# Optimization experiments

Hardware: AMD Instinct MI355X
Metric: run time of the kernel (lower is better)

Reference implementation:

```python
import jax, jax.numpy as jnp
import numpy as np

D_MODEL = 512
NUM_HEADS = 8
DEPTH = D_MODEL // NUM_HEADS


def setup_inputs() -> dict:
    key = jax.random.key(0)
    kx, kq, kk, kv, ko = jax.random.split(key, 5)
    scale = 1.0 / np.sqrt(D_MODEL)
    return {
        "x": jax.random.normal(kx, (4, 2048, D_MODEL), dtype=jnp.float32),
        "W_q": jax.random.normal(kq, (D_MODEL, D_MODEL), dtype=jnp.float32) * scale,
        "W_k": jax.random.normal(kk, (D_MODEL, D_MODEL), dtype=jnp.float32) * scale,
        "W_v": jax.random.normal(kv, (D_MODEL, D_MODEL), dtype=jnp.float32) * scale,
        "W_o": jax.random.normal(ko, (D_MODEL, D_MODEL), dtype=jnp.float32) * scale,
    }


def reference(x, W_q, W_k, W_v, W_o):
    B, S, _ = x.shape
    # nn.Linear with weight W: y = x @ W.T
    def split_heads(t):
        return t.reshape(B, S, NUM_HEADS, DEPTH).transpose(0, 2, 1, 3)  # [B,H,S,D]
    Q = split_heads(x @ W_q.T)
    K = split_heads(x @ W_k.T)
    V = split_heads(x @ W_v.T)
    b = -jnp.log(jnp.asarray(S, dtype=jnp.float32))  # -log(seq_len) bias
    inv_sqrt_dk = 1.0 / jnp.sqrt(jnp.asarray(DEPTH, dtype=jnp.float32))
    qk = jnp.einsum('bhqd,bhkd->bhqk', Q, K) * inv_sqrt_dk
    attn = jax.nn.sigmoid(qk + b)  # non-softmax sigmoid attention
    out = jnp.einsum('bhqk,bhkd->bhqd', attn, V)
    out = out.transpose(0, 2, 1, 3).reshape(B, S, D_MODEL)
    return out @ W_o.T
```

## Files before the change

kernel.cpp:

```cpp
#include <hip/hip_runtime.h>
#include <stdint.h>

typedef __bf16 bf16x8 __attribute__((ext_vector_type(8)));
typedef float f32x4 __attribute__((ext_vector_type(4)));
typedef unsigned short us4 __attribute__((ext_vector_type(4)));

#define SEQ 2048
#define NHEADS 8

#define GLOAD_LDS16(gp, lp)                                                        \
  __builtin_amdgcn_global_load_lds(                                                \
      (const __attribute__((address_space(1))) void*)(uintptr_t)(const void*)(gp), \
      (__attribute__((address_space(3))) void*)(uintptr_t)(void*)(lp), 16, 0, 0)

__device__ __forceinline__ unsigned short f2bf(float f) {
  unsigned int u = __builtin_bit_cast(unsigned int, f);
  u += 0x7fffu + ((u >> 16) & 1u);
  return (unsigned short)(u >> 16);
}

__global__ void cvt_kernel(const float* __restrict__ src,
                           unsigned short* __restrict__ dst, int n4) {
  int i = blockIdx.x * blockDim.x + threadIdx.x;
  if (i >= n4) return;
  float4 v = ((const float4*)src)[i];
  us4 o;
  o.x = f2bf(v.x); o.y = f2bf(v.y); o.z = f2bf(v.z); o.w = f2bf(v.w);
  ((us4*)dst)[i] = o;
}

__device__ __forceinline__ void gemm_tile_bt(const unsigned short* __restrict__ A,
                                             const unsigned short* __restrict__ B,
                                             int m0, int n0,
                                             unsigned short* As, unsigned short* Bs,
                                             f32x4 (&acc)[4][4]) {
  const int tid = threadIdx.x;
  const int w = tid >> 6, lane = tid & 63;
  const int wr = w >> 1, wc = w & 1;
  const int lrow = lane & 15, q = lane >> 4;
  const int snb = w * 32 + (lane >> 3);
  const int scb = lane & 7;

#pragma unroll
  for (int i = 0; i < 4; ++i)
#pragma unroll
    for (int j = 0; j < 4; ++j)
#pragma unroll
      for (int r = 0; r < 4; ++r) acc[i][j][r] = 0.f;

  for (int kt = 0; kt < 8; ++kt) {
    __syncthreads();
#pragma unroll
    for (int t = 0; t < 4; ++t) {
      int n = snb + t * 8;
      int cbg = scb ^ (n & 7);
      GLOAD_LDS16(A + (size_t)(m0 + n) * 512 + kt * 64 + cbg * 8,
                  As + (w * 32 + t * 8) * 64);
      GLOAD_LDS16(B + (size_t)(n0 + n) * 512 + kt * 64 + cbg * 8,
                  Bs + (w * 32 + t * 8) * 64);
    }
    __syncthreads();

    bf16x8 af[4][2], bfr[4][2];
#pragma unroll
    for (int i = 0; i < 4; ++i) {
      int m = wr * 64 + i * 16 + lrow;
#pragma unroll
      for (int kk = 0; kk < 2; ++kk) {
        int cb = (kk * 4 + q) ^ (m & 7);
        af[i][kk] = *(const bf16x8*)(As + m * 64 + cb * 8);
      }
    }
#pragma unroll
    for (int j = 0; j < 4; ++j) {
      int n = wc * 64 + j * 16 + lrow;
#pragma unroll
      for (int kk = 0; kk < 2; ++kk) {
        int cb = (kk * 4 + q) ^ (n & 7);
        bfr[j][kk] = *(const bf16x8*)(Bs + n * 64 + cb * 8);
      }
    }
#pragma unroll
    for (int i = 0; i < 4; ++i)
#pragma unroll
      for (int j = 0; j < 4; ++j) {
        acc[i][j] = __builtin_amdgcn_mfma_f32_16x16x32_bf16(af[i][0], bfr[j][0], acc[i][j], 0, 0, 0);
        acc[i][j] = __builtin_amdgcn_mfma_f32_16x16x32_bf16(af[i][1], bfr[j][1], acc[i][j], 0, 0, 0);
      }
  }
}

__global__ __launch_bounds__(256, 2) void qkv_kernel(
    const unsigned short* __restrict__ A, const unsigned short* __restrict__ Wq,
    const unsigned short* __restrict__ Wk, const unsigned short* __restrict__ Wv,
    unsigned short* __restrict__ Qo, unsigned short* __restrict__ Ko,
    unsigned short* __restrict__ Vto) {
  __shared__ unsigned short As[128 * 64];
  __shared__ unsigned short Bs[128 * 64];
  const int m0 = blockIdx.x * 128, n0 = blockIdx.y * 128, z = blockIdx.z;
  const unsigned short* Bp = (z == 0) ? Wq : (z == 1) ? Wk : Wv;
  f32x4 acc[4][4];
  gemm_tile_bt(A, Bp, m0, n0, As, Bs, acc);

  const int tid = threadIdx.x, w = tid >> 6, lane = tid & 63;
  const int wr = w >> 1, wc = w & 1, lcol = lane & 15, q = lane >> 4;
  if (z < 2) {
    unsigned short* outp = (z == 0) ? Qo : Ko;
#pragma unroll
    for (int i = 0; i < 4; ++i) {
      int gm0 = m0 + wr * 64 + i * 16 + q * 4;
#pragma unroll
      for (int j = 0; j < 4; ++j) {
        int gn = n0 + wc * 64 + j * 16 + lcol;
        int h = gn >> 6, d = gn & 63;
#pragma unroll
        for (int r = 0; r < 4; ++r) {
          int gm = gm0 + r;
          int b = gm >> 11, s = gm & 2047;
          outp[(((size_t)(b * NHEADS + h) * SEQ + s) << 6) + d] = f2bf(acc[i][j][r]);
        }
      }
    }
  } else {
#pragma unroll
    for (int i = 0; i < 4; ++i) {
      int gm0 = m0 + wr * 64 + i * 16 + q * 4;
      int b = gm0 >> 11, s0 = gm0 & 2047;
#pragma unroll
      for (int j = 0; j < 4; ++j) {
        int gn = n0 + wc * 64 + j * 16 + lcol;
        int h = gn >> 6, d = gn & 63;
        us4 v;
        v.x = f2bf(acc[i][j][0]); v.y = f2bf(acc[i][j][1]);
        v.z = f2bf(acc[i][j][2]); v.w = f2bf(acc[i][j][3]);
        *(us4*)(Vto + ((size_t)(b * NHEADS + h) * 64 + d) * SEQ + s0) = v;
      }
    }
  }
}

__global__ __launch_bounds__(256, 2) void attn_kernel(
    const unsigned short* __restrict__ Qw, const unsigned short* __restrict__ Kw,
    const unsigned short* __restrict__ Vtw, unsigned short* __restrict__ Ow) {
  __shared__ unsigned short lds[32768];
  unsigned short* Ks = lds;
  unsigned short* Vts = lds + 8192;
  unsigned short* Ps = lds + 16384;
  unsigned short* Qs = Ps;

  const int tid = threadIdx.x, w = tid >> 6, lane = tid & 63;
  const int wr = w >> 1, wc = w & 1, lrow = lane & 15, q = lane >> 4;
  const int bh = blockIdx.y, q0 = blockIdx.x * 128;
  const unsigned short* Qp = Qw + ((size_t)bh * SEQ + q0) * 64;
  const unsigned short* Kp = Kw + (size_t)bh * SEQ * 64;
  const unsigned short* Vp = Vtw + (size_t)bh * 64 * SEQ;

  const int snb = w * 32 + (lane >> 3), scb = lane & 7;
  const int vnb = w * 16 + (lane >> 4), vcb = lane & 15;

#pragma unroll
  for (int t = 0; t < 4; ++t) {
    int n = snb + t * 8;
    int cbg = scb ^ (n & 7);
    GLOAD_LDS16(Qp + (size_t)n * 64 + cbg * 8, Qs + (w * 32 + t * 8) * 64);
  }
  __syncthreads();

  bf16x8 qa[4][2];
#pragma unroll
  for (int i = 0; i < 4; ++i) {
    int m = wr * 64 + i * 16 + lrow;
#pragma unroll
    for (int kk = 0; kk < 2; ++kk) {
      int cb = (kk * 4 + q) ^ (m & 7);
      qa[i][kk] = *(const bf16x8*)(Qs + m * 64 + cb * 8);
    }
  }

  f32x4 oacc[4][2];
#pragma unroll
  for (int i = 0; i < 4; ++i)
#pragma unroll
    for (int j = 0; j < 2; ++j)
#pragma unroll
      for (int r = 0; r < 4; ++r) oacc[i][j][r] = 0.f;

  const float c1 = -0.18033688011112042f;

  for (int kt = 0; kt < 16; ++kt) {
    __syncthreads();
#pragma unroll
    for (int t = 0; t < 4; ++t) {
      int n = snb + t * 8;
      int cbg = scb ^ (n & 7);
      GLOAD_LDS16(Kp + (size_t)(kt * 128 + n) * 64 + cbg * 8, Ks + (w * 32 + t * 8) * 64);
    }
#pragma unroll
    for (int t = 0; t < 4; ++t) {
      int n = vnb + t * 4;
      int cbg = vcb ^ (n & 15);
      GLOAD_LDS16(Vp + (size_t)n * SEQ + kt * 128 + cbg * 8, Vts + (w * 16 + t * 4) * 128);
    }
    __syncthreads();

    f32x4 sacc[4][4];
#pragma unroll
    for (int i = 0; i < 4; ++i)
#pragma unroll
      for (int j = 0; j < 4; ++j)
#pragma unroll
        for (int r = 0; r < 4; ++r) sacc[i][j][r] = 0.f;
    bf16x8 kb[4][2];
#pragma unroll
    for (int j = 0; j < 4; ++j) {
      int n = wc * 64 + j * 16 + lrow;
#pragma unroll
      for (int kk = 0; kk < 2; ++kk) {
        int cb = (kk * 4 + q) ^ (n & 7);
        kb[j][kk] = *(const bf16x8*)(Ks + n * 64 + cb * 8);
      }
    }
#pragma unroll
    for (int i = 0; i < 4; ++i)
#pragma unroll
      for (int j = 0; j < 4; ++j) {
        sacc[i][j] = __builtin_amdgcn_mfma_f32_16x16x32_bf16(qa[i][0], kb[j][0], sacc[i][j], 0, 0, 0);
        sacc[i][j] = __builtin_amdgcn_mfma_f32_16x16x32_bf16(qa[i][1], kb[j][1], sacc[i][j], 0, 0, 0);
      }

#pragma unroll
    for (int i = 0; i < 4; ++i) {
      int prow0 = wr * 64 + i * 16 + q * 4;
#pragma unroll
      for (int j = 0; j < 4; ++j) {
        int pcol = wc * 64 + j * 16 + lrow;
        int cb = pcol >> 3, ci = pcol & 7;
#pragma unroll
        for (int r = 0; r < 4; ++r) {
          int prow = prow0 + r;
          float e = __builtin_amdgcn_exp2f(__builtin_fmaf(sacc[i][j][r], c1, 11.0f));
          float p = __builtin_amdgcn_rcpf(1.0f + e);
          Ps[prow * 128 + ((cb ^ (prow & 15)) * 8) + ci] = f2bf(p);
        }
      }
    }
    __syncthreads();

#pragma unroll
    for (int ks = 0; ks < 4; ++ks) {
      bf16x8 pa[4], vb[2];
#pragma unroll
      for (int i2 = 0; i2 < 4; ++i2) {
        int m = wr * 64 + i2 * 16 + lrow;
        int cb = (ks * 4 + q) ^ (m & 15);
        pa[i2] = *(const bf16x8*)(Ps + m * 128 + cb * 8);
      }
#pragma unroll
      for (int j2 = 0; j2 < 2; ++j2) {
        int n = wc * 32 + j2 * 16 + lrow;
        int cb = (ks * 4 + q) ^ (n & 15);
        vb[j2] = *(const bf16x8*)(Vts + n * 128 + cb * 8);
      }
#pragma unroll
      for (int i2 = 0; i2 < 4; ++i2)
#pragma unroll
        for (int j2 = 0; j2 < 2; ++j2)
          oacc[i2][j2] = __builtin_amdgcn_mfma_f32_16x16x32_bf16(pa[i2], vb[j2], oacc[i2][j2], 0, 0, 0);
    }
  }

  const int b = bh >> 3, h = bh & 7;
#pragma unroll
  for (int i2 = 0; i2 < 4; ++i2) {
#pragma unroll
    for (int j2 = 0; j2 < 2; ++j2) {
      int d = wc * 32 + j2 * 16 + lrow;
#pragma unroll
      for (int r = 0; r < 4; ++r) {
        int row = wr * 64 + i2 * 16 + q * 4 + r;
        int s = q0 + row;
        Ow[((size_t)(b * SEQ + s) * NHEADS + h) * 64 + d] = f2bf(oacc[i2][j2][r]);
      }
    }
  }
}

__global__ __launch_bounds__(256, 2) void oproj_kernel(
    const unsigned short* __restrict__ A, const unsigned short* __restrict__ Wo,
    float* __restrict__ out) {
  __shared__ unsigned short As[128 * 64];
  __shared__ unsigned short Bs[128 * 64];
  const int m0 = blockIdx.x * 128, n0 = blockIdx.y * 128;
  f32x4 acc[4][4];
  gemm_tile_bt(A, Wo, m0, n0, As, Bs, acc);

  const int tid = threadIdx.x, w = tid >> 6, lane = tid & 63;
  const int wr = w >> 1, wc = w & 1, lcol = lane & 15, q = lane >> 4;
#pragma unroll
  for (int i = 0; i < 4; ++i) {
    int gm0 = m0 + wr * 64 + i * 16 + q * 4;
#pragma unroll
    for (int j = 0; j < 4; ++j) {
      int gn = n0 + wc * 64 + j * 16 + lcol;
#pragma unroll
      for (int r = 0; r < 4; ++r)
        out[(size_t)(gm0 + r) * 512 + gn] = acc[i][j][r];
    }
  }
}

extern "C" void kernel_launch(void* const* d_in, const int* in_sizes, int n_in,
                              void* d_out, int out_size, void* d_ws, size_t ws_size,
                              hipStream_t stream) {
  const float* x = (const float*)d_in[0];
  const float* Wq = (const float*)d_in[1];
  const float* Wk = (const float*)d_in[2];
  const float* Wv = (const float*)d_in[3];
  const float* Wo = (const float*)d_in[4];
  float* out = (float*)d_out;
  char* ws = (char*)d_ws;

  unsigned short* xb  = (unsigned short*)(ws + 0);
  unsigned short* wqb = (unsigned short*)(ws + 8388608);
  unsigned short* wkb = (unsigned short*)(ws + 8912896);
  unsigned short* wvb = (unsigned short*)(ws + 9437184);
  unsigned short* wob = (unsigned short*)(ws + 9961472);
  unsigned short* Qw  = (unsigned short*)(ws + 10485760);
  unsigned short* Kw  = (unsigned short*)(ws + 18874368);
  unsigned short* Vtw = (unsigned short*)(ws + 27262976);
  unsigned short* Ow  = (unsigned short*)(ws + 35651584);

  cvt_kernel<<<4096, 256, 0, stream>>>(x, xb, 4194304 / 4);
  cvt_kernel<<<256, 256, 0, stream>>>(Wq, wqb, 262144 / 4);
  cvt_kernel<<<256, 256, 0, stream>>>(Wk, wkb, 262144 / 4);
  cvt_kernel<<<256, 256, 0, stream>>>(Wv, wvb, 262144 / 4);
  cvt_kernel<<<256, 256, 0, stream>>>(Wo, wob, 262144 / 4);

  qkv_kernel<<<dim3(64, 4, 3), 256, 0, stream>>>(xb, wqb, wkb, wvb, Qw, Kw, Vtw);
  attn_kernel<<<dim3(16, 32), 256, 0, stream>>>(Qw, Kw, Vtw, Ow);
  oproj_kernel<<<dim3(64, 4), 256, 0, stream>>>(Ow, wob, out);
}
```

Baseline: 177.0 us.

## Switch pipeline to fp16, shrink attention tiles, remap grid per XCD, merge weight casts

Converts every intermediate from bf16 to fp16, using packed RTZ conversion and fp16 MFMA. Q and K are now stored token-major with stride 512, and the QK GEMM is computed in transposed form. The attention kernel moves to 64-row query tiles with smaller LDS (P aliases K) to allow 4 blocks per CU, uses a 1-D grid mapped so each XCD handles contiguous heads for L2 reuse, and replaces the sigmoid's rcp with a scaled exp plus polynomial correction. The four weight conversion launches are merged into one. Risks include fp16 range/precision issues and the accuracy of the sigmoid approximation, which assumes the exponential term stays small.

```diff
diff --git a/kernel.cpp b/kernel.cpp
--- a/kernel.cpp
+++ b/kernel.cpp
@@ -1,9 +1,10 @@
 #include <hip/hip_runtime.h>
 #include <stdint.h>
 
-typedef __bf16 bf16x8 __attribute__((ext_vector_type(8)));
+typedef _Float16 f16x8 __attribute__((ext_vector_type(8)));
+typedef _Float16 f16x4 __attribute__((ext_vector_type(4)));
+typedef __fp16 h16x2 __attribute__((ext_vector_type(2)));
 typedef float f32x4 __attribute__((ext_vector_type(4)));
-typedef unsigned short us4 __attribute__((ext_vector_type(4)));
 
 #define SEQ 2048
 #define NHEADS 8
@@ -13,26 +14,36 @@
       (const __attribute__((address_space(1))) void*)(uintptr_t)(const void*)(gp), \
       (__attribute__((address_space(3))) void*)(uintptr_t)(void*)(lp), 16, 0, 0)
 
-__device__ __forceinline__ unsigned short f2bf(float f) {
-  unsigned int u = __builtin_bit_cast(unsigned int, f);
-  u += 0x7fffu + ((u >> 16) & 1u);
-  return (unsigned short)(u >> 16);
-}
-
-__global__ void cvt_kernel(const float* __restrict__ src,
-                           unsigned short* __restrict__ dst, int n4) {
+__device__ __forceinline__ f16x4 pack4(float a, float b, float c, float d) {
+  h16x2 lo = __builtin_amdgcn_cvt_pkrtz(a, b);
+  h16x2 hi = __builtin_amdgcn_cvt_pkrtz(c, d);
+  f16x4 o;
+  o.x = (_Float16)lo.x; o.y = (_Float16)lo.y;
+  o.z = (_Float16)hi.x; o.w = (_Float16)hi.y;
+  return o;
+}
+
+__global__ void cvt_x_kernel(const float* __restrict__ src,
+                             _Float16* __restrict__ dst, int n4) {
   int i = blockIdx.x * blockDim.x + threadIdx.x;
   if (i >= n4) return;
   float4 v = ((const float4*)src)[i];
-  us4 o;
-  o.x = f2bf(v.x); o.y = f2bf(v.y); o.z = f2bf(v.z); o.w = f2bf(v.w);
-  ((us4*)dst)[i] = o;
-}
-
-__device__ __forceinline__ void gemm_tile_bt(const unsigned short* __restrict__ A,
-                                             const unsigned short* __restrict__ B,
+  ((f16x4*)dst)[i] = pack4(v.x, v.y, v.z, v.w);
+}
+
+__global__ void cvt_w_kernel(const float* __restrict__ w0, const float* __restrict__ w1,
+                             const float* __restrict__ w2, const float* __restrict__ w3,
+                             _Float16* __restrict__ dst) {
+  const float* s = (blockIdx.y == 0) ? w0 : (blockIdx.y == 1) ? w1 : (blockIdx.y == 2) ? w2 : w3;
+  int i = blockIdx.x * 256 + threadIdx.x;
+  float4 v = ((const float4*)s)[i];
+  ((f16x4*)(dst + (size_t)blockIdx.y * 262144))[i] = pack4(v.x, v.y, v.z, v.w);
+}
+
+__device__ __forceinline__ void gemm_tile_bt(const _Float16* __restrict__ A,
+                                             const _Float16* __restrict__ B,
                                              int m0, int n0,
-                                             unsigned short* As, unsigned short* Bs,
+                                             _Float16* As, _Float16* Bs,
                                              f32x4 (&acc)[4][4]) {
   const int tid = threadIdx.x;
   const int w = tid >> 6, lane = tid & 63;
@@ -61,14 +72,14 @@
     }
     __syncthreads();
 
-    bf16x8 af[4][2], bfr[4][2];
+    f16x8 af[4][2], bfr[4][2];
 #pragma unroll
     for (int i = 0; i < 4; ++i) {
       int m = wr * 64 + i * 16 + lrow;
 #pragma unroll
       for (int kk = 0; kk < 2; ++kk) {
         int cb = (kk * 4 + q) ^ (m & 7);
-        af[i][kk] = *(const bf16x8*)(As + m * 64 + cb * 8);
+        af[i][kk] = *(const f16x8*)(As + m * 64 + cb * 8);
       }
     }
 #pragma unroll
@@ -77,160 +88,160 @@
 #pragma unroll
       for (int kk = 0; kk < 2; ++kk) {
         int cb = (kk * 4 + q) ^ (n & 7);
-        bfr[j][kk] = *(const bf16x8*)(Bs + n * 64 + cb * 8);
+        bfr[j][kk] = *(const f16x8*)(Bs + n * 64 + cb * 8);
       }
     }
 #pragma unroll
     for (int i = 0; i < 4; ++i)
 #pragma unroll
       for (int j = 0; j < 4; ++j) {
-        acc[i][j] = __builtin_amdgcn_mfma_f32_16x16x32_bf16(af[i][0], bfr[j][0], acc[i][j], 0, 0, 0);
-        acc[i][j] = __builtin_amdgcn_mfma_f32_16x16x32_bf16(af[i][1], bfr[j][1], acc[i][j], 0, 0, 0);
+        acc[i][j] = __builtin_amdgcn_mfma_f32_16x16x32_f16(af[i][0], bfr[j][0], acc[i][j], 0, 0, 0);
+        acc[i][j] = __builtin_amdgcn_mfma_f32_16x16x32_f16(af[i][1], bfr[j][1], acc[i][j], 0, 0, 0);
       }
   }
 }
 
 __global__ __launch_bounds__(256, 2) void qkv_kernel(
-    const unsigned short* __restrict__ A, const unsigned short* __restrict__ Wq,
-    const unsigned short* __restrict__ Wk, const unsigned short* __restrict__ Wv,
-    unsigned short* __restrict__ Qo, unsigned short* __restrict__ Ko,
-    unsigned short* __restrict__ Vto) {
-  __shared__ unsigned short As[128 * 64];
-  __shared__ unsigned short Bs[128 * 64];
-  const int m0 = blockIdx.x * 128, n0 = blockIdx.y * 128, z = blockIdx.z;
-  const unsigned short* Bp = (z == 0) ? Wq : (z == 1) ? Wk : Wv;
+    const _Float16* __restrict__ xb, const _Float16* __restrict__ Wq,
+    const _Float16* __restrict__ Wk, const _Float16* __restrict__ Wv,
+    _Float16* __restrict__ Qo, _Float16* __restrict__ Ko, _Float16* __restrict__ Vto) {
+  __shared__ _Float16 As[128 * 64];
+  __shared__ _Float16 Bs[128 * 64];
+  const int z = blockIdx.z;
   f32x4 acc[4][4];
-  gemm_tile_bt(A, Bp, m0, n0, As, Bs, acc);
-
   const int tid = threadIdx.x, w = tid >> 6, lane = tid & 63;
   const int wr = w >> 1, wc = w & 1, lcol = lane & 15, q = lane >> 4;
+
   if (z < 2) {
-    unsigned short* outp = (z == 0) ? Qo : Ko;
+    const int m0 = blockIdx.y * 128;
+    const int n0 = blockIdx.x * 128;
+    gemm_tile_bt((z == 0) ? Wq : Wk, xb, m0, n0, As, Bs, acc);
+    _Float16* outp = (z == 0) ? Qo : Ko;
 #pragma unroll
     for (int i = 0; i < 4; ++i) {
-      int gm0 = m0 + wr * 64 + i * 16 + q * 4;
-#pragma unroll
-      for (int j = 0; j < 4; ++j) {
-        int gn = n0 + wc * 64 + j * 16 + lcol;
-        int h = gn >> 6, d = gn & 63;
-#pragma unroll
-        for (int r = 0; r < 4; ++r) {
-          int gm = gm0 + r;
-          int b = gm >> 11, s = gm & 2047;
-          outp[(((size_t)(b * NHEADS + h) * SEQ + s) << 6) + d] = f2bf(acc[i][j][r]);
-        }
+      int c0 = m0 + wr * 64 + i * 16 + q * 4;
+#pragma unroll
+      for (int j = 0; j < 4; ++j) {
+        int s = n0 + wc * 64 + j * 16 + lcol;
+        *(f16x4*)(outp + (size_t)s * 512 + c0) =
+            pack4(acc[i][j][0], acc[i][j][1], acc[i][j][2], acc[i][j][3]);
       }
     }
   } else {
+    const int m0 = blockIdx.x * 128;
+    const int n0 = blockIdx.y * 128;
+    gemm_tile_bt(xb, Wv, m0, n0, As, Bs, acc);
 #pragma unroll
     for (int i = 0; i < 4; ++i) {
-      int gm0 = m0 + wr * 64 + i * 16 + q * 4;
-      int b = gm0 >> 11, s0 = gm0 & 2047;
-#pragma unroll
-      for (int j = 0; j < 4; ++j) {
-        int gn = n0 + wc * 64 + j * 16 + lcol;
-        int h = gn >> 6, d = gn & 63;
-        us4 v;
-        v.x = f2bf(acc[i][j][0]); v.y = f2bf(acc[i][j][1]);
-        v.z = f2bf(acc[i][j][2]); v.w = f2bf(acc[i][j][3]);
-        *(us4*)(Vto + ((size_t)(b * NHEADS + h) * 64 + d) * SEQ + s0) = v;
-      }
-    }
-  }
-}
-
-__global__ __launch_bounds__(256, 2) void attn_kernel(
-    const unsigned short* __restrict__ Qw, const unsigned short* __restrict__ Kw,
-    const unsigned short* __restrict__ Vtw, unsigned short* __restrict__ Ow) {
-  __shared__ unsigned short lds[32768];
-  unsigned short* Ks = lds;
-  unsigned short* Vts = lds + 8192;
-  unsigned short* Ps = lds + 16384;
-  unsigned short* Qs = Ps;
+      int s0 = m0 + wr * 64 + i * 16 + q * 4;
+      int b = s0 >> 11, sl = s0 & 2047;
+#pragma unroll
+      for (int j = 0; j < 4; ++j) {
+        int c = n0 + wc * 64 + j * 16 + lcol;
+        int h = c >> 6, d = c & 63;
+        *(f16x4*)(Vto + ((size_t)((b * NHEADS + h) * 64 + d)) * SEQ + sl) =
+            pack4(acc[i][j][0], acc[i][j][1], acc[i][j][2], acc[i][j][3]);
+      }
+    }
+  }
+}
+
+__global__ __launch_bounds__(256, 4) void attn_kernel(
+    const _Float16* __restrict__ Qw, const _Float16* __restrict__ Kw,
+    const _Float16* __restrict__ Vtw, _Float16* __restrict__ Ow) {
+  __shared__ _Float16 lds[20480];
+  _Float16* Ks = lds;
+  _Float16* Qs = lds + 8192;
+  _Float16* Vts = lds + 12288;
+  _Float16* Ps = lds;
 
   const int tid = threadIdx.x, w = tid >> 6, lane = tid & 63;
   const int wr = w >> 1, wc = w & 1, lrow = lane & 15, q = lane >> 4;
-  const int bh = blockIdx.y, q0 = blockIdx.x * 128;
-  const unsigned short* Qp = Qw + ((size_t)bh * SEQ + q0) * 64;
-  const unsigned short* Kp = Kw + (size_t)bh * SEQ * 64;
-  const unsigned short* Vp = Vtw + (size_t)bh * 64 * SEQ;
-
-  const int snb = w * 32 + (lane >> 3), scb = lane & 7;
-  const int vnb = w * 16 + (lane >> 4), vcb = lane & 15;
-
-#pragma unroll
-  for (int t = 0; t < 4; ++t) {
-    int n = snb + t * 8;
-    int cbg = scb ^ (n & 7);
-    GLOAD_LDS16(Qp + (size_t)n * 64 + cbg * 8, Qs + (w * 32 + t * 8) * 64);
+
+  const int L = blockIdx.x;
+  const int xcd = L & 7, slot = L >> 3;
+  const int bh = xcd * 4 + (slot >> 5), qt = slot & 31;
+  const int b = bh >> 3, h = bh & 7;
+
+  const _Float16* Qp = Qw + ((size_t)(b * SEQ + qt * 64)) * 512 + h * 64;
+  const _Float16* Kp = Kw + ((size_t)b * SEQ) * 512 + h * 64;
+  const _Float16* Vp = Vtw + (size_t)bh * 64 * SEQ;
+
+#pragma unroll
+  for (int t = 0; t < 2; ++t) {
+    int n = w * 16 + t * 8 + (lane >> 3);
+    int cbg = (lane & 7) ^ (n & 7);
+    GLOAD_LDS16(Qp + (size_t)n * 512 + cbg * 8, Qs + (w * 16 + t * 8) * 64);
   }
   __syncthreads();
 
-  bf16x8 qa[4][2];
-#pragma unroll
-  for (int i = 0; i < 4; ++i) {
-    int m = wr * 64 + i * 16 + lrow;
+  f16x8 qa[2][2];
+#pragma unroll
+  for (int i = 0; i < 2; ++i) {
+    int m = wr * 32 + i * 16 + lrow;
 #pragma unroll
     for (int kk = 0; kk < 2; ++kk) {
       int cb = (kk * 4 + q) ^ (m & 7);
-      qa[i][kk] = *(const bf16x8*)(Qs + m * 64 + cb * 8);
-    }
-  }
-
-  f32x4 oacc[4][2];
-#pragma unroll
-  for (int i = 0; i < 4; ++i)
+      qa[i][kk] = *(const f16x8*)(Qs + m * 64 + cb * 8);
+    }
+  }
+
+  f32x4 oacc[2][2];
+#pragma unroll
+  for (int i = 0; i < 2; ++i)
 #pragma unroll
     for (int j = 0; j < 2; ++j)
 #pragma unroll
       for (int r = 0; r < 4; ++r) oacc[i][j][r] = 0.f;
 
-  const float c1 = -0.18033688011112042f;
+  const float c1 = 0.18033688011112042f;
 
   for (int kt = 0; kt < 16; ++kt) {
     __syncthreads();
 #pragma unroll
     for (int t = 0; t < 4; ++t) {
-      int n = snb + t * 8;
-      int cbg = scb ^ (n & 7);
-      GLOAD_LDS16(Kp + (size_t)(kt * 128 + n) * 64 + cbg * 8, Ks + (w * 32 + t * 8) * 64);
+      int n = w * 32 + t * 8 + (lane >> 3);
+      int cbg = (lane & 7) ^ (n & 7);
+      GLOAD_LDS16(Kp + (size_t)(kt * 128 + n) * 512 + cbg * 8, Ks + (w * 32 + t * 8) * 64);
     }
 #pragma unroll
     for (int t = 0; t < 4; ++t) {
-      int n = vnb + t * 4;
-      int cbg = vcb ^ (n & 15);
-      GLOAD_LDS16(Vp + (size_t)n * SEQ + kt * 128 + cbg * 8, Vts + (w * 16 + t * 4) * 128);
-    }
-    __syncthreads();
-
-    f32x4 sacc[4][4];
-#pragma unroll
-    for (int i = 0; i < 4; ++i)
+      int nv = w * 16 + t * 4 + (lane >> 4);
+      int cbg = (lane & 15) ^ (nv & 15);
+      GLOAD_LDS16(Vp + (size_t)nv * SEQ + kt * 128 + cbg * 8, Vts + (w * 16 + t * 4) * 128);
+    }
+    __syncthreads();
+
+    f32x4 sacc[2][4];
+#pragma unroll
+    for (int i = 0; i < 2; ++i)
 #pragma unroll
       for (int j = 0; j < 4; ++j)
 #pragma unroll
         for (int r = 0; r < 4; ++r) sacc[i][j][r] = 0.f;
-    bf16x8 kb[4][2];
+    f16x8 kb[4][2];
 #pragma unroll
     for (int j = 0; j < 4; ++j) {
       int n = wc * 64 + j * 16 + lrow;
 #pragma unroll
       for (int kk = 0; kk < 2; ++kk) {
         int cb = (kk * 4 + q) ^ (n & 7);
-        kb[j][kk] = *(const bf16x8*)(Ks + n * 64 + cb * 8);
-      }
-    }
-#pragma unroll
-    for (int i = 0; i < 4; ++i)
-#pragma unroll
-      for (int j = 0; j < 4; ++j) {
-        sacc[i][j] = __builtin_amdgcn_mfma_f32_16x16x32_bf16(qa[i][0], kb[j][0], sacc[i][j], 0, 0, 0);
-        sacc[i][j] = __builtin_amdgcn_mfma_f32_16x16x32_bf16(qa[i][1], kb[j][1], sacc[i][j], 0, 0, 0);
-      }
-
-#pragma unroll
-    for (int i = 0; i < 4; ++i) {
-      int prow0 = wr * 64 + i * 16 + q * 4;
+        kb[j][kk] = *(const f16x8*)(Ks + n * 64 + cb * 8);
+      }
+    }
+#pragma unroll
+    for (int i = 0; i < 2; ++i)
+#pragma unroll
+      for (int j = 0; j < 4; ++j) {
+        sacc[i][j] = __builtin_amdgcn_mfma_f32_16x16x32_f16(qa[i][0], kb[j][0], sacc[i][j], 0, 0, 0);
+        sacc[i][j] = __builtin_amdgcn_mfma_f32_16x16x32_f16(qa[i][1], kb[j][1], sacc[i][j], 0, 0, 0);
+      }
+
+    __syncthreads();
+
+#pragma unroll
+    for (int i = 0; i < 2; ++i) {
+      int prow0 = wr * 32 + i * 16 + q * 4;
 #pragma unroll
       for (int j = 0; j < 4; ++j) {
         int pcol = wc * 64 + j * 16 + lrow;
@@ -238,9 +249,10 @@
 #pragma unroll
         for (int r = 0; r < 4; ++r) {
           int prow = prow0 + r;
-          float e = __builtin_amdgcn_exp2f(__builtin_fmaf(sacc[i][j][r], c1, 11.0f));
-          float p = __builtin_amdgcn_rcpf(1.0f + e);
-          Ps[prow * 128 + ((cb ^ (prow & 15)) * 8) + ci] = f2bf(p);
+          float wp = __builtin_amdgcn_exp2f(__builtin_fmaf(sacc[i][j][r], c1, -1.0f));
+          float u = wp * -0.0009765625f;
+          float zz = __builtin_fmaf(u, __builtin_fmaf(u, 1.0f + u, 1.0f), 1.0f);
+          Ps[prow * 128 + ((cb ^ (prow & 15)) << 3) + ci] = (_Float16)(wp * zz);
         }
       }
     }
@@ -248,48 +260,47 @@
 
 #pragma unroll
     for (int ks = 0; ks < 4; ++ks) {
-      bf16x8 pa[4], vb[2];
-#pragma unroll
-      for (int i2 = 0; i2 < 4; ++i2) {
-        int m = wr * 64 + i2 * 16 + lrow;
+      f16x8 pa[2], vb[2];
+#pragma unroll
+      for (int i2 = 0; i2 < 2; ++i2) {
+        int m = wr * 32 + i2 * 16 + lrow;
         int cb = (ks * 4 + q) ^ (m & 15);
-        pa[i2] = *(const bf16x8*)(Ps + m * 128 + cb * 8);
+        pa[i2] = *(const f16x8*)(Ps + m * 128 + cb * 8);
       }
 #pragma unroll
       for (int j2 = 0; j2 < 2; ++j2) {
         int n = wc * 32 + j2 * 16 + lrow;
         int cb = (ks * 4 + q) ^ (n & 15);
-        vb[j2] = *(const bf16x8*)(Vts + n * 128 + cb * 8);
-      }
-#pragma unroll
-      for (int i2 = 0; i2 < 4; ++i2)
+        vb[j2] = *(const f16x8*)(Vts + n * 128 + cb * 8);
+      }
+#pragma unroll
+      for (int i2 = 0; i2 < 2; ++i2)
 #pragma unroll
         for (int j2 = 0; j2 < 2; ++j2)
-          oacc[i2][j2] = __builtin_amdgcn_mfma_f32_16x16x32_bf16(pa[i2], vb[j2], oacc[i2][j2], 0, 0, 0);
-    }
-  }
-
-  const int b = bh >> 3, h = bh & 7;
-#pragma unroll
-  for (int i2 = 0; i2 < 4; ++i2) {
+          oacc[i2][j2] = __builtin_amdgcn_mfma_f32_16x16x32_f16(pa[i2], vb[j2], oacc[i2][j2], 0, 0, 0);
+    }
+  }
+
+#pragma unroll
+  for (int i2 = 0; i2 < 2; ++i2) {
 #pragma unroll
     for (int j2 = 0; j2 < 2; ++j2) {
       int d = wc * 32 + j2 * 16 + lrow;
 #pragma unroll
       for (int r = 0; r < 4; ++r) {
-        int row = wr * 64 + i2 * 16 + q * 4 + r;
-        int s = q0 + row;
-        Ow[((size_t)(b * SEQ + s) * NHEADS + h) * 64 + d] = f2bf(oacc[i2][j2][r]);
+        int s = qt * 64 + wr * 32 + i2 * 16 + q * 4 + r;
+        Ow[((size_t)(b * SEQ + s)) * 512 + h * 64 + d] =
+            (_Float16)(oacc[i2][j2][r] * 0.0009765625f);
       }
     }
   }
 }
 
 __global__ __launch_bounds__(256, 2) void oproj_kernel(
-    const unsigned short* __restrict__ A, const unsigned short* __restrict__ Wo,
+    const _Float16* __restrict__ A, const _Float16* __restrict__ Wo,
     float* __restrict__ out) {
-  __shared__ unsigned short As[128 * 64];
-  __shared__ unsigned short Bs[128 * 64];
+  __shared__ _Float16 As[128 * 64];
+  __shared__ _Float16 Bs[128 * 64];
   const int m0 = blockIdx.x * 128, n0 = blockIdx.y * 128;
   f32x4 acc[4][4];
   gemm_tile_bt(A, Wo, m0, n0, As, Bs, acc);
@@ -320,23 +331,22 @@
   float* out = (float*)d_out;
   char* ws = (char*)d_ws;
 
-  unsigned short* xb  = (unsigned short*)(ws + 0);
-  unsigned short* wqb = (unsigned short*)(ws + 8388608);
-  unsigned short* wkb = (unsigned short*)(ws + 8912896);
-  unsigned short* wvb = (unsigned short*)(ws + 9437184);
-  unsigned short* wob = (unsigned short*)(ws + 9961472);
-  unsigned short* Qw  = (unsigned short*)(ws + 10485760);
-  unsigned short* Kw  = (unsigned short*)(ws + 18874368);
-  unsigned short* Vtw = (unsigned short*)(ws + 27262976);
-  unsigned short* Ow  = (unsigned short*)(ws + 35651584);
-
-  cvt_kernel<<<4096, 256, 0, stream>>>(x, xb, 4194304 / 4);
-  cvt_kernel<<<256, 256, 0, stream>>>(Wq, wqb, 262144 / 4);
-  cvt_kernel<<<256, 256, 0, stream>>>(Wk, wkb, 262144 / 4);
-  cvt_kernel<<<256, 256, 0, stream>>>(Wv, wvb, 262144 / 4);
-  cvt_kernel<<<256, 256, 0, stream>>>(Wo, wob, 262144 / 4);
-
-  qkv_kernel<<<dim3(64, 4, 3), 256, 0, stream>>>(xb, wqb, wkb, wvb, Qw, Kw, Vtw);
-  attn_kernel<<<dim3(16, 32), 256, 0, stream>>>(Qw, Kw, Vtw, Ow);
-  oproj_kernel<<<dim3(64, 4), 256, 0, stream>>>(Ow, wob, out);
-}
+  _Float16* xh = (_Float16*)(ws + 0);
+  _Float16* wh = (_Float16*)(ws + 8388608);
+  _Float16* Qw = (_Float16*)(ws + 10485760);
+  _Float16* Kw = (_Float16*)(ws + 18874368);
+  _Float16* Vtw = (_Float16*)(ws + 27262976);
+  _Float16* Ow = (_Float16*)(ws + 35651584);
+
+  _Float16* wqh = wh;
+  _Float16* wkh = wh + 262144;
+  _Float16* wvh = wh + 524288;
+  _Float16* woh = wh + 786432;
+
+  cvt_x_kernel<<<4096, 256, 0, stream>>>(x, xh, 1048576);
+  cvt_w_kernel<<<dim3(256, 4), 256, 0, stream>>>(Wq, Wk, Wv, Wo, wh);
+
+  qkv_kernel<<<dim3(64, 4, 3), 256, 0, stream>>>(xh, wqh, wkh, wvh, Qw, Kw, Vtw);
+  attn_kernel<<<1024, 256, 0, stream>>>(Qw, Kw, Vtw, Ow);
+  oproj_kernel<<<dim3(64, 4), 256, 0, stream>>>(Ow, woh, out);
+}
```

Measured after the change: 199.6 us. 12.7% more time.
